# Kernel tuning notes

Hardware: AMD Instinct MI355X
Metric: run time of the kernel (lower is better)

Reference implementation:

```python
import jax, jax.numpy as jnp
import numpy as np

# Dimensions
B, LQ, HQ, HKV, D = 4, 512, 16, 8, 128          # seqs, q tokens/seq, q heads, kv heads, head dim
BLOCK_SIZE, BLOCKS_PER_SEQ, NUM_BLOCKS = 256, 8, 64  # paged KV-cache geometry
CTX = BLOCK_SIZE * BLOCKS_PER_SEQ                # cached tokens per seq (full blocks, rem=0)
LK = CTX + LQ                                    # keys per seq = cache + current step
DIFF_BLOCK = 128                                 # diffusion block: bidirectional inside, causal across
SCALE = 1.0 / float(np.sqrt(D))


def _make_allow_mask():
    # True = allowed to attend. All cached tokens visible; within the current
    # step, query attends up to the end of its own diffusion block (block-causal,
    # intra-block bidirectional) -- the semantics described in the module docstring.
    qi = jnp.arange(LQ)
    kj = jnp.arange(LK)
    limit = CTX + ((qi // DIFF_BLOCK) + 1) * DIFF_BLOCK   # [LQ]
    m = kj[None, :] < limit[:, None]                      # [LQ, LK]
    return jnp.broadcast_to(m[None], (B, LQ, LK))


def setup_inputs() -> dict:
    key = jax.random.key(0)
    ks = jax.random.split(key, 6)
    q = jax.random.normal(ks[0], (B, LQ, HQ, D), jnp.float32)
    k = jax.random.normal(ks[1], (B, LQ, HKV, D), jnp.float32)
    v = jax.random.normal(ks[2], (B, LQ, HKV, D), jnp.float32)
    k_cache = jax.random.normal(ks[3], (NUM_BLOCKS, BLOCK_SIZE, HKV, D), jnp.float32)
    v_cache = jax.random.normal(ks[4], (NUM_BLOCKS, BLOCK_SIZE, HKV, D), jnp.float32)
    # distinct physical block slots per sequence (as a paged allocator would give)
    block_tables = jax.random.permutation(ks[5], NUM_BLOCKS)[: B * BLOCKS_PER_SEQ]
    block_tables = block_tables.reshape(B, BLOCKS_PER_SEQ).astype(jnp.int32)
    allow_mask = _make_allow_mask()
    return dict(q=q, k=k, v=v, k_cache=k_cache, v_cache=v_cache,
                block_tables=block_tables, allow_mask=allow_mask)


def reference(q, k, v, k_cache, v_cache, block_tables, allow_mask):
    rep = HQ // HKV
    # paged gather: [B, nblk, blk, Hkv, D] -> [B, CTX, Hkv, D]
    K_ctx = k_cache[block_tables].reshape(B, CTX, HKV, D)
    V_ctx = v_cache[block_tables].reshape(B, CTX, HKV, D)
    K_all = jnp.concatenate([K_ctx, k], axis=1)   # [B, LK, Hkv, D]
    V_all = jnp.concatenate([V_ctx, v], axis=1)
    # GQA: repeat_interleave kv heads to q heads
    K_all = jnp.repeat(K_all, rep, axis=2)        # [B, LK, Hq, D]
    V_all = jnp.repeat(V_all, rep, axis=2)
    scores = jnp.einsum('bqhd,bkhd->bhqk', q * SCALE, K_all)  # [B, Hq, LQ, LK]
    neg = jnp.finfo(scores.dtype).min
    scores = jnp.where(allow_mask[:, None, :, :], scores, neg)
    attn = jax.nn.softmax(scores, axis=-1)
    return jnp.einsum('bhqk,bkhd->bqhd', attn, V_all)         # [B, LQ, Hq, D]
```

## Files before the change

### kernel.cpp

```cpp
#include <hip/hip_runtime.h>
#include <hip/hip_bf16.h>


#define B_    4
#define LQ_   512
#define HQ_   16
#define HKV_  8
#define D_    128
#define BLKSZ_ 256
#define BPS_  8
#define CTX_  2048
#define DIFFB_ 128
#define KT_   64
#define SCALE_ 0.08838834764831845f

typedef __attribute__((ext_vector_type(4))) float f32x4;
typedef __attribute__((ext_vector_type(8))) short bf16x8;
typedef __attribute__((ext_vector_type(2))) unsigned u32x2;

__device__ __forceinline__ unsigned cvt_pk2(float a, float b) {
  union { __hip_bfloat162 h; unsigned u; } x;
  x.h = __float22bfloat162_rn(float2{a, b});
  return x.u;
}
union bf8u { bf16x8 v; unsigned u[4]; };

__device__ __forceinline__ int kidx(int kv, int d) {
  return kv * 128 + ((((d >> 3) ^ kv) & 15) << 3) + (d & 7);
}
__device__ __forceinline__ int vidx(int d, int p) {
  return d * 64 + ((((p >> 3) ^ d ^ (d >> 3)) & 7) << 3) + (p & 7);
}
__device__ __forceinline__ int pk32(int w) {
  return (((w >> 2) & 3) << 3) | (((w >> 4) & 1) << 2) | (w & 3);
}

__global__ __launch_bounds__(768)
void block_attn_kernel(const float* __restrict__ qg,
                       const float* __restrict__ kcur,
                       const float* __restrict__ vcur,
                       const float* __restrict__ kcache,
                       const float* __restrict__ vcache,
                       const int*   __restrict__ btab,
                       float*       __restrict__ out) {
  const int blk  = blockIdx.x;
  const int hkv  = blk & 7;
  const int b    = (blk >> 3) & 3;
  const int qb   = blk >> 5;
  const int tid  = threadIdx.x;
  const int lane = tid & 63;
  const int wave = tid >> 6;
  const int lo   = lane & 15;
  const int hi   = lane >> 4;
  const int nt   = (CTX_ + (qb / 2 + 1) * DIFFB_) / KT_;

  __shared__ __align__(16) char smem[65536];
  __shared__ float ms[8][16], ls[8][16];
  float* Os = (float*)smem;

  if (wave < 8) {
    const int kvh  = wave & 1;
    const int g    = wave >> 1;
    const int hq    = hkv * 2 + (g >> 1);
    const int qrow0 = qb * 64 + (g & 1) * 32;

    bf16x8 qf[2][4];
#pragma unroll
    for (int sub = 0; sub < 2; ++sub) {
      const float* qr = qg + ((size_t)((b * LQ_ + qrow0 + sub * 16 + lo)) * HQ_ + hq) * D_;
#pragma unroll
      for (int db = 0; db < 4; ++db) {
        const int d0 = db * 32 + hi * 8;
        f32x4 a  = *(const f32x4*)(qr + d0);
        f32x4 c4 = *(const f32x4*)(qr + d0 + 4);
        bf8u f;
        f.u[0] = cvt_pk2(a[0] * SCALE_, a[1] * SCALE_);
        f.u[1] = cvt_pk2(a[2] * SCALE_, a[3] * SCALE_);
        f.u[2] = cvt_pk2(c4[0] * SCALE_, c4[1] * SCALE_);
        f.u[3] = cvt_pk2(c4[2] * SCALE_, c4[3] * SCALE_);
        qf[sub][db] = f.v;
      }
    }

    f32x4 oacc[2][8];
#pragma unroll
    for (int s = 0; s < 2; ++s)
#pragma unroll
      for (int i = 0; i < 8; ++i) oacc[s][i] = (f32x4){0.f, 0.f, 0.f, 0.f};
    float mrow[2] = {-1e30f, -1e30f}, lrow[2] = {0.f, 0.f};

    __syncthreads();

    for (int t = 0; t < nt; ++t) {
      const short* Kb = (const short*)(smem + (t & 1) * 16384);
      const short* Vb = (const short*)(smem + 32768 + (t & 1) * 16384);

      f32x4 sacc[2][2];
#pragma unroll
      for (int s = 0; s < 2; ++s)
#pragma unroll
        for (int cs = 0; cs < 2; ++cs) sacc[s][cs] = (f32x4){0.f, 0.f, 0.f, 0.f};
#pragma unroll
      for (int cs = 0; cs < 2; ++cs) {
#pragma unroll
        for (int db = 0; db < 4; ++db) {
          bf16x8 kf = *(const bf16x8*)&Kb[kidx(kvh * 32 + cs * 16 + lo,
                                               db * 32 + hi * 8)];
          sacc[0][cs] = __builtin_amdgcn_mfma_f32_16x16x32_bf16(kf, qf[0][db], sacc[0][cs], 0, 0, 0);
          sacc[1][cs] = __builtin_amdgcn_mfma_f32_16x16x32_bf16(kf, qf[1][db], sacc[1][cs], 0, 0, 0);
        }
      }

      bf16x8 pa[2];
#pragma unroll
      for (int sub = 0; sub < 2; ++sub) {
        float m0 = fmaxf(fmaxf(sacc[sub][0][0], sacc[sub][0][1]),
                         fmaxf(sacc[sub][0][2], sacc[sub][0][3]));
        float m1 = fmaxf(fmaxf(sacc[sub][1][0], sacc[sub][1][1]),
                         fmaxf(sacc[sub][1][2], sacc[sub][1][3]));
        float mx = fmaxf(m0, m1);
        mx = fmaxf(mx, __shfl_xor(mx, 16));
        mx = fmaxf(mx, __shfl_xor(mx, 32));
        const bool keep = __all(mx - mrow[sub] <= 8.0f);
        const float mnew = keep ? mrow[sub] : fmaxf(mrow[sub], mx);
        float rs = 0.f;
#pragma unroll
        for (int cs = 0; cs < 2; ++cs)
#pragma unroll
          for (int i = 0; i < 4; ++i) {
            const float p = __expf(sacc[sub][cs][i] - mnew);
            sacc[sub][cs][i] = p;
            rs += p;
          }
        rs += __shfl_xor(rs, 16);
        rs += __shfl_xor(rs, 32);
        if (keep) {
          lrow[sub] += rs;
        } else {
          const float sc = __expf(mrow[sub] - mnew);
          lrow[sub] = lrow[sub] * sc + rs;
          mrow[sub] = mnew;
#pragma unroll
          for (int dt = 0; dt < 8; ++dt) oacc[sub][dt] *= sc;
        }
        bf8u p;
        p.u[0] = cvt_pk2(sacc[sub][0][0], sacc[sub][0][1]);
        p.u[1] = cvt_pk2(sacc[sub][0][2], sacc[sub][0][3]);
        p.u[2] = cvt_pk2(sacc[sub][1][0], sacc[sub][1][1]);
        p.u[3] = cvt_pk2(sacc[sub][1][2], sacc[sub][1][3]);
        pa[sub] = p.v;
      }

#pragma unroll
      for (int dt = 0; dt < 8; ++dt) {
        bf16x8 vf = *(const bf16x8*)&Vb[vidx(dt * 16 + lo, kvh * 32 + hi * 8)];
        oacc[0][dt] = __builtin_amdgcn_mfma_f32_16x16x32_bf16(vf, pa[0], oacc[0][dt], 0, 0, 0);
        oacc[1][dt] = __builtin_amdgcn_mfma_f32_16x16x32_bf16(vf, pa[1], oacc[1][dt], 0, 0, 0);
      }

      __syncthreads();
    }

    if (kvh == 1) {
#pragma unroll
      for (int sub = 0; sub < 2; ++sub) {
#pragma unroll
        for (int dt = 0; dt < 8; ++dt)
          *(f32x4*)&Os[(size_t)(g * 32 + sub * 16 + lo) * 128 + dt * 16 + hi * 4] =
              oacc[sub][dt];
        if (hi == 0) { ms[g * 2 + sub][lo] = mrow[sub]; ls[g * 2 + sub][lo] = lrow[sub]; }
      }
    }
    __syncthreads();
    if (kvh == 0) {
#pragma unroll
      for (int sub = 0; sub < 2; ++sub) {
        const float m1 = ms[g * 2 + sub][lo], l1 = ls[g * 2 + sub][lo];
        const float mstar = fmaxf(mrow[sub], m1);
        const float a0 = __expf(mrow[sub] - mstar);
        const float a1 = __expf(m1 - mstar);
        const float linv = 1.f / (lrow[sub] * a0 + l1 * a1);
        float* orow = out + ((size_t)(b * LQ_ + qrow0 + sub * 16 + lo) * HQ_ + hq) * D_;
#pragma unroll
        for (int dt = 0; dt < 8; ++dt) {
          f32x4 o1 = *(const f32x4*)&Os[(size_t)(g * 32 + sub * 16 + lo) * 128 + dt * 16 + hi * 4];
          f32x4 o = (oacc[sub][dt] * a0 + o1 * a1) * linv;
          *(f32x4*)(orow + dt * 16 + hi * 4) = o;
        }
      }
    }
  } else {
    const int pid = tid & 255;
    const int cK  = pid >> 4;
    const int e   = pid & 15;
    const int qd  = pid >> 4;
    const int dc  = pid & 15;
    const int r0v = qd * 4;
    const int d0v = dc * 8;
    const int P0v = (r0v & 32) + pk32(r0v & 31);
    f32x4 kreg[4][2], vreg[4][2];

    auto issue_loads = [&](int t) {
      const int kbase = t * KT_;
      const float *kb_, *vb_;
      if (kbase < CTX_) {
        const int pb = btab[b * BPS_ + (kbase >> 8)];
        const size_t base = ((size_t)(pb * BLKSZ_ + (kbase & 255)) * HKV_ + hkv) * D_;
        kb_ = kcache + base; vb_ = vcache + base;
      } else {
        const size_t base = ((size_t)(b * LQ_ + (kbase - CTX_)) * HKV_ + hkv) * D_;
        kb_ = kcur + base;  vb_ = vcur + base;
      }
      const size_t rs = (size_t)HKV_ * D_;
#pragma unroll
      for (int i = 0; i < 4; ++i) {
        const float* kr = kb_ + (size_t)(cK + 16 * i) * rs + e * 8;
        kreg[i][0] = *(const f32x4*)(kr);
        kreg[i][1] = *(const f32x4*)(kr + 4);
      }
#pragma unroll
      for (int m = 0; m < 4; ++m) {
        const float* vr = vb_ + (size_t)(r0v + m) * rs + d0v;
        vreg[m][0] = *(const f32x4*)(vr);
        vreg[m][1] = *(const f32x4*)(vr + 4);
      }
    };

    auto write_lds = [&](int bsel) {
      short* Kb = (short*)(smem + bsel * 16384);
      short* Vb = (short*)(smem + 32768 + bsel * 16384);
#pragma unroll
      for (int i = 0; i < 4; ++i) {
        bf8u f;
        f.u[0] = cvt_pk2(kreg[i][0][0], kreg[i][0][1]);
        f.u[1] = cvt_pk2(kreg[i][0][2], kreg[i][0][3]);
        f.u[2] = cvt_pk2(kreg[i][1][0], kreg[i][1][1]);
        f.u[3] = cvt_pk2(kreg[i][1][2], kreg[i][1][3]);
        *(bf16x8*)&Kb[kidx(cK + 16 * i, e * 8)] = f.v;
      }
#pragma unroll
      for (int j = 0; j < 8; ++j) {
        u32x2 w;
        w[0] = cvt_pk2(vreg[0][j >> 2][j & 3], vreg[1][j >> 2][j & 3]);
        w[1] = cvt_pk2(vreg[2][j >> 2][j & 3], vreg[3][j >> 2][j & 3]);
        *(u32x2*)&Vb[vidx(d0v + j, P0v)] = w;
      }
    };

    issue_loads(0);
    write_lds(0);
    if (nt > 1) issue_loads(1);
    asm volatile("s_waitcnt lgkmcnt(0)" ::: "memory");
    __builtin_amdgcn_s_barrier();

    for (int t = 0; t < nt; ++t) {
      if (t + 1 < nt) write_lds((t + 1) & 1);
      if (t + 2 < nt) issue_loads(t + 2);
      asm volatile("s_waitcnt lgkmcnt(0)" ::: "memory");
      __builtin_amdgcn_s_barrier();
    }
    __builtin_amdgcn_s_barrier();
  }
}

extern "C" void kernel_launch(void* const* d_in, const int* in_sizes, int n_in,
                              void* d_out, int out_size, void* d_ws, size_t ws_size,
                              hipStream_t stream) {
  (void)in_sizes; (void)n_in; (void)out_size; (void)d_ws; (void)ws_size;
  const float* q      = (const float*)d_in[0];
  const float* k      = (const float*)d_in[1];
  const float* v      = (const float*)d_in[2];
  const float* kcache = (const float*)d_in[3];
  const float* vcache = (const float*)d_in[4];
  const int*   btab   = (const int*)d_in[5];
  float* out = (float*)d_out;

  block_attn_kernel<<<dim3(B_ * HKV_ * (LQ_ / 64)), dim3(768), 0, stream>>>(
      q, k, v, kcache, vcache, btab, out);
}
```

Baseline: 81.18 us.

## Use four compute waves each handling 64 query rows to raise K/V fragment reuse

Cuts the compute waves from 8 to 4. Each wave now processes four 16-row query tiles instead of two, so every K and V fragment loaded from LDS feeds four MFMAs rather than two. The block drops to 512 threads (4 compute plus 4 loader waves) with launch bounds set for two blocks per CU, which is meant to halve LDS read traffic per MFMA and let blocks overlap. In exchange each wave holds more accumulator and Q registers and has less wave-level parallelism inside the block. Register pressure under the 2-block bound could cause spills, and the Os staging buffer now spans the full 64 KB of smem.

```diff
diff --git a/kernel.cpp b/kernel.cpp
--- a/kernel.cpp
+++ b/kernel.cpp
@@ -35,7 +35,7 @@
   return (((w >> 2) & 3) << 3) | (((w >> 4) & 1) << 2) | (w & 3);
 }
 
-__global__ __launch_bounds__(768)
+__global__ __launch_bounds__(512, 2)
 void block_attn_kernel(const float* __restrict__ qg,
                        const float* __restrict__ kcur,
                        const float* __restrict__ vcur,
@@ -58,16 +58,16 @@
   __shared__ float ms[8][16], ls[8][16];
   float* Os = (float*)smem;
 
-  if (wave < 8) {
+  if (wave < 4) {
     const int kvh  = wave & 1;
-    const int g    = wave >> 1;
-    const int hq    = hkv * 2 + (g >> 1);
-    const int qrow0 = qb * 64 + (g & 1) * 32;
-
-    bf16x8 qf[2][4];
-#pragma unroll
-    for (int sub = 0; sub < 2; ++sub) {
-      const float* qr = qg + ((size_t)((b * LQ_ + qrow0 + sub * 16 + lo)) * HQ_ + hq) * D_;
+    const int pair = wave >> 1;
+    const int hq   = hkv * 2 + pair;
+    const int qrow0 = qb * 64;
+
+    bf16x8 qf[4][4];
+#pragma unroll
+    for (int qt = 0; qt < 4; ++qt) {
+      const float* qr = qg + ((size_t)((b * LQ_ + qrow0 + qt * 16 + lo)) * HQ_ + hq) * D_;
 #pragma unroll
       for (int db = 0; db < 4; ++db) {
         const int d0 = db * 32 + hi * 8;
@@ -78,16 +78,17 @@
         f.u[1] = cvt_pk2(a[2] * SCALE_, a[3] * SCALE_);
         f.u[2] = cvt_pk2(c4[0] * SCALE_, c4[1] * SCALE_);
         f.u[3] = cvt_pk2(c4[2] * SCALE_, c4[3] * SCALE_);
-        qf[sub][db] = f.v;
-      }
-    }
-
-    f32x4 oacc[2][8];
-#pragma unroll
-    for (int s = 0; s < 2; ++s)
-#pragma unroll
-      for (int i = 0; i < 8; ++i) oacc[s][i] = (f32x4){0.f, 0.f, 0.f, 0.f};
-    float mrow[2] = {-1e30f, -1e30f}, lrow[2] = {0.f, 0.f};
+        qf[qt][db] = f.v;
+      }
+    }
+
+    f32x4 oacc[8][4];
+#pragma unroll
+    for (int dt = 0; dt < 8; ++dt)
+#pragma unroll
+      for (int qt = 0; qt < 4; ++qt) oacc[dt][qt] = (f32x4){0.f, 0.f, 0.f, 0.f};
+    float mrow[4] = {-1e30f, -1e30f, -1e30f, -1e30f};
+    float lrow[4] = {0.f, 0.f, 0.f, 0.f};
 
     __syncthreads();
 
@@ -95,67 +96,72 @@
       const short* Kb = (const short*)(smem + (t & 1) * 16384);
       const short* Vb = (const short*)(smem + 32768 + (t & 1) * 16384);
 
-      f32x4 sacc[2][2];
-#pragma unroll
-      for (int s = 0; s < 2; ++s)
-#pragma unroll
-        for (int cs = 0; cs < 2; ++cs) sacc[s][cs] = (f32x4){0.f, 0.f, 0.f, 0.f};
+      f32x4 sacc[4][2];
+#pragma unroll
+      for (int qt = 0; qt < 4; ++qt) {
+        sacc[qt][0] = (f32x4){0.f, 0.f, 0.f, 0.f};
+        sacc[qt][1] = (f32x4){0.f, 0.f, 0.f, 0.f};
+      }
 #pragma unroll
       for (int cs = 0; cs < 2; ++cs) {
 #pragma unroll
         for (int db = 0; db < 4; ++db) {
           bf16x8 kf = *(const bf16x8*)&Kb[kidx(kvh * 32 + cs * 16 + lo,
                                                db * 32 + hi * 8)];
-          sacc[0][cs] = __builtin_amdgcn_mfma_f32_16x16x32_bf16(kf, qf[0][db], sacc[0][cs], 0, 0, 0);
-          sacc[1][cs] = __builtin_amdgcn_mfma_f32_16x16x32_bf16(kf, qf[1][db], sacc[1][cs], 0, 0, 0);
+#pragma unroll
+          for (int qt = 0; qt < 4; ++qt)
+            sacc[qt][cs] = __builtin_amdgcn_mfma_f32_16x16x32_bf16(
+                kf, qf[qt][db], sacc[qt][cs], 0, 0, 0);
         }
       }
 
-      bf16x8 pa[2];
-#pragma unroll
-      for (int sub = 0; sub < 2; ++sub) {
-        float m0 = fmaxf(fmaxf(sacc[sub][0][0], sacc[sub][0][1]),
-                         fmaxf(sacc[sub][0][2], sacc[sub][0][3]));
-        float m1 = fmaxf(fmaxf(sacc[sub][1][0], sacc[sub][1][1]),
-                         fmaxf(sacc[sub][1][2], sacc[sub][1][3]));
+      bf16x8 pa[4];
+#pragma unroll
+      for (int qt = 0; qt < 4; ++qt) {
+        float m0 = fmaxf(fmaxf(sacc[qt][0][0], sacc[qt][0][1]),
+                         fmaxf(sacc[qt][0][2], sacc[qt][0][3]));
+        float m1 = fmaxf(fmaxf(sacc[qt][1][0], sacc[qt][1][1]),
+                         fmaxf(sacc[qt][1][2], sacc[qt][1][3]));
         float mx = fmaxf(m0, m1);
         mx = fmaxf(mx, __shfl_xor(mx, 16));
         mx = fmaxf(mx, __shfl_xor(mx, 32));
-        const bool keep = __all(mx - mrow[sub] <= 8.0f);
-        const float mnew = keep ? mrow[sub] : fmaxf(mrow[sub], mx);
+        const bool keep = __all(mx - mrow[qt] <= 8.0f);
+        const float mnew = keep ? mrow[qt] : fmaxf(mrow[qt], mx);
         float rs = 0.f;
 #pragma unroll
         for (int cs = 0; cs < 2; ++cs)
 #pragma unroll
           for (int i = 0; i < 4; ++i) {
-            const float p = __expf(sacc[sub][cs][i] - mnew);
-            sacc[sub][cs][i] = p;
+            const float p = __expf(sacc[qt][cs][i] - mnew);
+            sacc[qt][cs][i] = p;
             rs += p;
           }
         rs += __shfl_xor(rs, 16);
         rs += __shfl_xor(rs, 32);
         if (keep) {
-          lrow[sub] += rs;
+          lrow[qt] += rs;
         } else {
-          const float sc = __expf(mrow[sub] - mnew);
-          lrow[sub] = lrow[sub] * sc + rs;
-          mrow[sub] = mnew;
-#pragma unroll
-          for (int dt = 0; dt < 8; ++dt) oacc[sub][dt] *= sc;
+          const float sc = __expf(mrow[qt] - mnew);
+          lrow[qt] = lrow[qt] * sc + rs;
+          mrow[qt] = mnew;
+#pragma unroll
+          for (int dt = 0; dt < 8; ++dt) oacc[dt][qt] *= sc;
         }
         bf8u p;
-        p.u[0] = cvt_pk2(sacc[sub][0][0], sacc[sub][0][1]);
-        p.u[1] = cvt_pk2(sacc[sub][0][2], sacc[sub][0][3]);
-        p.u[2] = cvt_pk2(sacc[sub][1][0], sacc[sub][1][1]);
-        p.u[3] = cvt_pk2(sacc[sub][1][2], sacc[sub][1][3]);
-        pa[sub] = p.v;
+        p.u[0] = cvt_pk2(sacc[qt][0][0], sacc[qt][0][1]);
+        p.u[1] = cvt_pk2(sacc[qt][0][2], sacc[qt][0][3]);
+        p.u[2] = cvt_pk2(sacc[qt][1][0], sacc[qt][1][1]);
+        p.u[3] = cvt_pk2(sacc[qt][1][2], sacc[qt][1][3]);
+        pa[qt] = p.v;
       }
 
 #pragma unroll
       for (int dt = 0; dt < 8; ++dt) {
         bf16x8 vf = *(const bf16x8*)&Vb[vidx(dt * 16 + lo, kvh * 32 + hi * 8)];
-        oacc[0][dt] = __builtin_amdgcn_mfma_f32_16x16x32_bf16(vf, pa[0], oacc[0][dt], 0, 0, 0);
-        oacc[1][dt] = __builtin_amdgcn_mfma_f32_16x16x32_bf16(vf, pa[1], oacc[1][dt], 0, 0, 0);
+#pragma unroll
+        for (int qt = 0; qt < 4; ++qt)
+          oacc[dt][qt] = __builtin_amdgcn_mfma_f32_16x16x32_bf16(
+              vf, pa[qt], oacc[dt][qt], 0, 0, 0);
       }
 
       __syncthreads();
@@ -163,28 +169,28 @@
 
     if (kvh == 1) {
 #pragma unroll
-      for (int sub = 0; sub < 2; ++sub) {
+      for (int qt = 0; qt < 4; ++qt) {
 #pragma unroll
         for (int dt = 0; dt < 8; ++dt)
-          *(f32x4*)&Os[(size_t)(g * 32 + sub * 16 + lo) * 128 + dt * 16 + hi * 4] =
-              oacc[sub][dt];
-        if (hi == 0) { ms[g * 2 + sub][lo] = mrow[sub]; ls[g * 2 + sub][lo] = lrow[sub]; }
+          *(f32x4*)&Os[(size_t)(pair * 64 + qt * 16 + lo) * 128 + dt * 16 + hi * 4] =
+              oacc[dt][qt];
+        if (hi == 0) { ms[pair * 4 + qt][lo] = mrow[qt]; ls[pair * 4 + qt][lo] = lrow[qt]; }
       }
     }
     __syncthreads();
     if (kvh == 0) {
 #pragma unroll
-      for (int sub = 0; sub < 2; ++sub) {
-        const float m1 = ms[g * 2 + sub][lo], l1 = ls[g * 2 + sub][lo];
-        const float mstar = fmaxf(mrow[sub], m1);
-        const float a0 = __expf(mrow[sub] - mstar);
+      for (int qt = 0; qt < 4; ++qt) {
+        const float m1 = ms[pair * 4 + qt][lo], l1 = ls[pair * 4 + qt][lo];
+        const float mstar = fmaxf(mrow[qt], m1);
+        const float a0 = __expf(mrow[qt] - mstar);
         const float a1 = __expf(m1 - mstar);
-        const float linv = 1.f / (lrow[sub] * a0 + l1 * a1);
-        float* orow = out + ((size_t)(b * LQ_ + qrow0 + sub * 16 + lo) * HQ_ + hq) * D_;
+        const float linv = 1.f / (lrow[qt] * a0 + l1 * a1);
+        float* orow = out + ((size_t)(b * LQ_ + qrow0 + qt * 16 + lo) * HQ_ + hq) * D_;
 #pragma unroll
         for (int dt = 0; dt < 8; ++dt) {
-          f32x4 o1 = *(const f32x4*)&Os[(size_t)(g * 32 + sub * 16 + lo) * 128 + dt * 16 + hi * 4];
-          f32x4 o = (oacc[sub][dt] * a0 + o1 * a1) * linv;
+          f32x4 o1 = *(const f32x4*)&Os[(size_t)(pair * 64 + qt * 16 + lo) * 128 + dt * 16 + hi * 4];
+          f32x4 o = (oacc[dt][qt] * a0 + o1 * a1) * linv;
           *(f32x4*)(orow + dt * 16 + hi * 4) = o;
         }
       }
@@ -275,6 +281,6 @@
   const int*   btab   = (const int*)d_in[5];
   float* out = (float*)d_out;
 
-  block_attn_kernel<<<dim3(B_ * HKV_ * (LQ_ / 64)), dim3(768), 0, stream>>>(
+  block_attn_kernel<<<dim3(B_ * HKV_ * (LQ_ / 64)), dim3(512), 0, stream>>>(
       q, k, v, kcache, vcache, btab, out);
 }
```

New measurement: 124.0 us. 1.53x slower.
